# Kernel optimization log

Hardware: AMD Instinct MI355X
Metric: run time of the kernel (lower is better)

## Reference

```python
import jax, jax.numpy as jnp
import numpy as np

CUTOFF = 5.0
EPS = 1e-7
N = 50000
L = 160.0


def _cart3(a, b, c):
    # cartesian product of ranges [-a..a] x [-b..b] x [-c..c], row-major like torch.cartesian_prod
    A, B, C = np.meshgrid(np.arange(-a, a + 1), np.arange(-b, b + 1), np.arange(-c, c + 1), indexing='ij')
    return np.stack([A.ravel(), B.ravel(), C.ravel()], axis=1)


def wrap_positions(positions, cell):
    scaled = positions @ jnp.linalg.inv(cell) + EPS
    scaled = scaled % 1.0 - EPS
    return scaled @ cell


def setup_inputs() -> dict:
    key = jax.random.key(0)
    positions = jax.random.uniform(key, (N, 3), dtype=jnp.float32) * L
    cell = jnp.eye(3, dtype=jnp.float32) * L
    return {"positions": positions, "cell": cell}


def reference(positions, cell):
    wrapped = wrap_positions(positions, cell)

    cell_np = np.asarray(cell, dtype=np.float64)
    norm_a = np.linalg.norm(np.cross(cell_np[1], cell_np[2]))
    norm_b = np.linalg.norm(np.cross(cell_np[2], cell_np[0]))
    norm_c = np.linalg.norm(np.cross(cell_np[0], cell_np[1]))
    volume = float(np.dot(cell_np[0], np.cross(cell_np[1], cell_np[2])))
    pa = int(np.ceil(CUTOFF * norm_a / volume))
    pb = int(np.ceil(CUTOFF * norm_b / volume))
    pc = int(np.ceil(CUTOFF * norm_c / volume))

    pad_mat = jnp.asarray(_cart3(pa, pb, pc), dtype=positions.dtype)  # [P,3]
    P = pad_mat.shape[0]
    n = wrapped.shape[0]

    # replicate atoms into all periodic images: index k -> atom k//P, image k%P
    padded_pos = (wrapped[:, None, :] + pad_mat @ cell).reshape(-1, 3)  # [n*P,3]
    padded_cpos = jnp.floor(padded_pos / CUTOFF).astype(jnp.int32)
    corner = padded_cpos.min(axis=0)
    padded_cpos = padded_cpos - corner
    shap = np.asarray(padded_cpos.max(axis=0)) + 1
    num_cells = int(shap.prod())
    count_vec = jnp.asarray([int(shap[1] * shap[2]), int(shap[2]), 1], dtype=jnp.int32)

    padded_cind = (padded_cpos * count_vec).sum(axis=1)  # linear cell id per padded atom
    padded_gind = jnp.arange(n * P, dtype=jnp.int32) + 1  # 1-based so 0 == empty slot
    padded_rind = jnp.repeat(jnp.arange(n, dtype=jnp.int32), P)  # real-atom id of each image

    atom_cpos = jnp.floor(wrapped / CUTOFF).astype(jnp.int32) - corner
    disp = jnp.asarray(_cart3(1, 1, 1), dtype=jnp.int32)  # 27-cell stencil
    atom_cnind = ((atom_cpos[:, None, :] + disp) * count_vec).sum(axis=-1)  # [n,27]

    # stable sort by cell id, then within-cell rank (== torch unique_consecutive bookkeeping)
    cind_np = np.asarray(padded_cind)
    order = np.argsort(cind_np, kind='stable')
    sorted_cind = cind_np[order]
    _, counts = np.unique(sorted_cind, return_counts=True)
    max_anum = int(counts.max())
    starts = np.repeat(np.cumsum(counts) - counts, counts)
    ranks = np.arange(sorted_cind.shape[0]) - starts

    gci = jnp.zeros((num_cells, max_anum, 2), dtype=jnp.int32)
    gci = gci.at[sorted_cind, ranks, 0].set(padded_gind[order])
    gci = gci.at[sorted_cind, ranks, 1].set(padded_rind[order])

    atom_nind = gci[atom_cnind]  # [n,27,max_anum,2]
    occ = np.asarray(atom_nind[..., 0])
    pair_i, neigh, jslot = np.nonzero(occ)
    pair_jp = occ[pair_i, neigh, jslot] - 1  # index into padded_pos
    pair_j = np.asarray(atom_nind[..., 1])[pair_i, neigh, jslot]

    pair_diff = padded_pos[pair_jp] - wrapped[pair_i]
    pair_dist = jnp.linalg.norm(pair_diff, axis=1)
    mask = np.asarray((pair_dist < CUTOFF) & (pair_dist > 0.01))
    keep = np.nonzero(mask)[0]

    pairs = jnp.stack([jnp.asarray(pair_i, jnp.int32), jnp.asarray(pair_j, jnp.int32)], axis=1)
    return pairs[keep], pair_diff[keep], pair_dist[keep]
```

## Files before the change

kernel.cpp:

```cpp
#include <hip/hip_runtime.h>


#define CUTOFF 5.0f
#define WEPS   1e-7f
#define PIMG   27
#define G      36
#define NCELLS (G*G*G)
#define SLOT   16
#define NT1    256
#define NB2    2048
#define NT2    256
#define JPT    3
#define CAP    16
#define CSTR   17
#define BCAP   512
#define IMAX   0x7FFFFFFF
#define PRUNE2 25.001f


__device__ __forceinline__ void inv_diag3(const float* __restrict__ cell, float inv[9]) {
  float c[9];
#pragma unroll
  for (int i = 0; i < 9; i++) c[i] = cell[i];
  float a00=c[0],a01=c[1],a02=c[2],a10=c[3],a11=c[4],a12=c[5],a20=c[6],a21=c[7],a22=c[8];
  float m00 = __fsub_rn(__fmul_rn(a11,a22), __fmul_rn(a12,a21));
  float m01 = __fsub_rn(__fmul_rn(a10,a22), __fmul_rn(a12,a20));
  float m02 = __fsub_rn(__fmul_rn(a10,a21), __fmul_rn(a11,a20));
  float det = __fadd_rn(__fsub_rn(__fmul_rn(a00,m00), __fmul_rn(a01,m01)), __fmul_rn(a02,m02));
  inv[0] = __fdiv_rn(m00, det);
  inv[1] = __fdiv_rn(__fsub_rn(__fmul_rn(a02,a21), __fmul_rn(a01,a22)), det);
  inv[2] = __fdiv_rn(__fsub_rn(__fmul_rn(a01,a12), __fmul_rn(a02,a11)), det);
  inv[3] = __fdiv_rn(__fsub_rn(__fmul_rn(a12,a20), __fmul_rn(a10,a22)), det);
  inv[4] = __fdiv_rn(__fsub_rn(__fmul_rn(a00,a22), __fmul_rn(a02,a20)), det);
  inv[5] = __fdiv_rn(__fsub_rn(__fmul_rn(a02,a10), __fmul_rn(a00,a12)), det);
  inv[6] = __fdiv_rn(m02, det);
  inv[7] = __fdiv_rn(__fsub_rn(__fmul_rn(a01,a20), __fmul_rn(a00,a21)), det);
  inv[8] = __fdiv_rn(__fsub_rn(__fmul_rn(a00,a11), __fmul_rn(a01,a10)), det);
}

__device__ __forceinline__ int axis_opts(float w, float cdiag, int* pcomp, int* cellv,
                                         float* shv) {
  int cc = (int)floorf(__fdiv_rn(w, CUTOFF));
  int k = 0;
  if (cc >= 29) {
    float wp = __fsub_rn(w, cdiag);
    int c2 = (int)floorf(__fdiv_rn(wp, CUTOFF)) + 2;
    if ((unsigned)c2 < G) { pcomp[k] = 0; cellv[k] = c2; shv[k] = __fsub_rn(0.0f, cdiag); k++; }
  }
  pcomp[k] = 1; cellv[k] = cc + 2; shv[k] = 0.0f; k++;
  if (cc <= 2) {
    float wp = __fadd_rn(w, cdiag);
    int c2 = (int)floorf(__fdiv_rn(wp, CUTOFF)) + 2;
    if ((unsigned)c2 < G) { pcomp[k] = 2; cellv[k] = c2; shv[k] = cdiag; k++; }
  }
  return k;
}

__device__ __forceinline__ bool dist_ok(float4 f, float4 w) {
  float ax = __fsub_rn(f.x, w.x), ay = __fsub_rn(f.y, w.y), az = __fsub_rn(f.z, w.z);
  float d = __fsqrt_rn(__fadd_rn(__fadd_rn(__fmul_rn(ax, ax), __fmul_rn(ay, ay)),
                                 __fmul_rn(az, az)));
  return (d < CUTOFF && d > 0.01f);
}

__device__ __forceinline__ unsigned match_mask(const float4* __restrict__ cdata,
                                               int base, int cnt, float4 w) {
  unsigned mask = 0;
  for (int q = 0; q < cnt; q++)
    if (dist_ok(cdata[base + q], w)) mask |= 1u << q;
  return mask;
}

__device__ __forceinline__ int pick_min_t(const float4* __restrict__ cdata, int base,
                                          unsigned mask) {
  int bq = -1, bt = IMAX;
  for (unsigned m2 = mask; m2; m2 &= m2 - 1) {
    int q = __builtin_ctz(m2);
    int t = __float_as_int(cdata[base + q].w);
    if (t < bt) { bt = t; bq = q; }
  }
  return bq;
}

__device__ __forceinline__ float axis_q(float w, int c) {
  float lo = (float)((c - 2) * 5);
  float t = w - lo;
  float v = fmaxf(fmaxf(-t, t - 5.0f), 0.0f);
  return v * v;
}

__device__ __forceinline__ void cswap(int& a, int& b) {
  int lo = min(a, b), hi = max(a, b);
  a = lo; b = hi;
}

__device__ __forceinline__ int exscan256(int v, int* lds, int* total) {
  int tid = threadIdx.x, lane = tid & 63, wave = tid >> 6;
  int x = v;
#pragma unroll
  for (int off = 1; off < 64; off <<= 1) {
    int y = __shfl_up(x, off);
    if (lane >= off) x += y;
  }
  if (lane == 63) lds[wave] = x;
  __syncthreads();
  if (wave == 0) {
    int wv = (lane < 4) ? lds[lane] : 0;
#pragma unroll
    for (int off = 1; off < 4; off <<= 1) {
      int y = __shfl_up(wv, off);
      if (lane >= off) wv += y;
    }
    if (lane < 4) lds[lane] = wv;
  }
  __syncthreads();
  int wbase = (wave == 0) ? 0 : lds[wave - 1];
  *total = lds[3];
  __syncthreads();
  return wbase + x - v;
}

__device__ __forceinline__ int exscan1024(int v, int* lds, int* total) {
  int tid = threadIdx.x, lane = tid & 63, wave = tid >> 6;
  int x = v;
#pragma unroll
  for (int off = 1; off < 64; off <<= 1) {
    int y = __shfl_up(x, off);
    if (lane >= off) x += y;
  }
  if (lane == 63) lds[wave] = x;
  __syncthreads();
  if (wave == 0) {
    int wv = (lane < 16) ? lds[lane] : 0;
#pragma unroll
    for (int off = 1; off < 16; off <<= 1) {
      int y = __shfl_up(wv, off);
      if (lane >= off) wv += y;
    }
    if (lane < 16) lds[lane] = wv;
  }
  __syncthreads();
  int wbase = (wave == 0) ? 0 : lds[wave - 1];
  *total = lds[15];
  __syncthreads();
  return wbase + x - v;
}

__global__ void __launch_bounds__(NT1)
k_build(const float* __restrict__ pos, const float* __restrict__ cell,
        int* __restrict__ fill, float4* __restrict__ wrapped,
        float4* __restrict__ cdata, int n) {
  const int ai = blockIdx.x * NT1 + threadIdx.x;
  if (ai >= n) return;
  float inv[9];
  inv_diag3(cell, inv);
  float px = pos[3*ai], py = pos[3*ai+1], pz = pos[3*ai+2];
  float m[3];
#pragma unroll
  for (int col = 0; col < 3; col++) {
    float s = __fadd_rn(__fadd_rn(__fmul_rn(px, inv[col]), __fmul_rn(py, inv[3+col])),
                        __fmul_rn(pz, inv[6+col]));
    s = __fadd_rn(s, WEPS);
    float t = __fsub_rn(s, floorf(s));
    m[col] = __fsub_rn(t, WEPS);
  }
  float wx = __fadd_rn(__fadd_rn(__fmul_rn(m[0], cell[0]), __fmul_rn(m[1], cell[3])),
                       __fmul_rn(m[2], cell[6]));
  float wy = __fadd_rn(__fadd_rn(__fmul_rn(m[0], cell[1]), __fmul_rn(m[1], cell[4])),
                       __fmul_rn(m[2], cell[7]));
  float wz = __fadd_rn(__fadd_rn(__fmul_rn(m[0], cell[2]), __fmul_rn(m[1], cell[5])),
                       __fmul_rn(m[2], cell[8]));
  wrapped[ai] = make_float4(wx, wy, wz, 0.0f);
  int px_[2], py_[2], pz_[2], cx_[2], cy_[2], cz_[2];
  float sx_[2], sy_[2], sz_[2];
  int nx = axis_opts(wx, cell[0], px_, cx_, sx_);
  int ny = axis_opts(wy, cell[4], py_, cy_, sy_);
  int nz = axis_opts(wz, cell[8], pz_, cz_, sz_);
  for (int a = 0; a < nx; a++)
    for (int b = 0; b < ny; b++)
      for (int c = 0; c < nz; c++) {
        int cid = (cx_[a] * G + cy_[b]) * G + cz_[c];
        int p = (px_[a] * 3 + py_[b]) * 3 + pz_[c];
        int slot = atomicAdd(&fill[cid], 1);
        if (slot < SLOT)
          cdata[cid * SLOT + slot] =
              make_float4(__fadd_rn(wx, sx_[a]), __fadd_rn(wy, sy_[b]),
                          __fadd_rn(wz, sz_[c]), __int_as_float(ai * PIMG + p));
      }
}

__global__ void __launch_bounds__(NT2)
k_pair(const float4* __restrict__ wrapped, const int* __restrict__ fill,
       const float4* __restrict__ cdata, int2* __restrict__ paddr,
       int* __restrict__ blockSum, int n) {
  __shared__ int lds[8];
  __shared__ int pcache[NT2 * CSTR];
  const int tid = threadIdx.x, blk = blockIdx.x;
  const int n27 = n * PIMG;
  const int tbase = (blk * NT2 + tid) * JPT;
  const int i0 = min(tbase, n27 - 1) / PIMG;
  const int i1 = min(tbase + JPT - 1, n27 - 1) / PIMG;
  const float4 w0 = wrapped[i0];
  const float4 w1 = wrapped[i1];
  const int cx0 = (int)floorf(__fdiv_rn(w0.x, CUTOFF)) + 2;
  const int cy0 = (int)floorf(__fdiv_rn(w0.y, CUTOFF)) + 2;
  const int cz0 = (int)floorf(__fdiv_rn(w0.z, CUTOFF)) + 2;
  const int cx1 = (int)floorf(__fdiv_rn(w1.x, CUTOFF)) + 2;
  const int cy1 = (int)floorf(__fdiv_rn(w1.y, CUTOFF)) + 2;
  const int cz1 = (int)floorf(__fdiv_rn(w1.z, CUTOFF)) + 2;
  int bases[JPT], cnts[JPT];
#pragma unroll
  for (int j = 0; j < JPT; j++) {
    int idx = tbase + j;
    bool valid = idx < n27;
    int ic = valid ? idx / PIMG : i0;
    int s27 = valid ? idx - ic * PIMG : 0;
    bool a0 = (ic == i0);
    int ix = s27 / 9, iy = (s27 / 3) % 3, iz = s27 % 3;
    float wxs = a0 ? w0.x : w1.x, wys = a0 ? w0.y : w1.y, wzs = a0 ? w0.z : w1.z;
    int cx = (a0 ? cx0 : cx1) + ix - 1;
    int cy = (a0 ? cy0 : cy1) + iy - 1;
    int cz = (a0 ? cz0 : cz1) + iz - 1;
    float ps = axis_q(wxs, cx) + axis_q(wys, cy) + axis_q(wzs, cz);
    bool keep = valid && (ps <= PRUNE2);
    int cid = (cx * G + cy) * G + cz;
    bases[j] = cid * SLOT;
    cnts[j] = keep ? min(fill[cid], SLOT) : 0;
  }
  int tcnt = 0, c0 = 0;
#pragma unroll
  for (int j = 0; j < JPT; j++) {
    bool a0 = (tbase + j) < (i0 + 1) * PIMG;
    float4 w = a0 ? w0 : w1;
    int base = bases[j], cnt = cnts[j];
    if (cnt > 0) {
      if (cnt <= 4) {
        float4 f0 = cdata[base + 0];
        float4 f1 = cdata[base + 1];
        float4 f2 = cdata[base + 2];
        float4 f3 = cdata[base + 3];
        int a = (cnt > 0 && dist_ok(f0, w)) ? (__float_as_int(f0.w) * 16 + 0) : IMAX;
        int b = (cnt > 1 && dist_ok(f1, w)) ? (__float_as_int(f1.w) * 16 + 1) : IMAX;
        int c = (cnt > 2 && dist_ok(f2, w)) ? (__float_as_int(f2.w) * 16 + 2) : IMAX;
        int d = (cnt > 3 && dist_ok(f3, w)) ? (__float_as_int(f3.w) * 16 + 3) : IMAX;
        cswap(a, b); cswap(c, d); cswap(a, c); cswap(b, d); cswap(b, c);
        if (a != IMAX) { if (tcnt < CAP) pcache[tid * CSTR + tcnt] = base + (a & 15); tcnt++; }
        if (b != IMAX) { if (tcnt < CAP) pcache[tid * CSTR + tcnt] = base + (b & 15); tcnt++; }
        if (c != IMAX) { if (tcnt < CAP) pcache[tid * CSTR + tcnt] = base + (c & 15); tcnt++; }
        if (d != IMAX) { if (tcnt < CAP) pcache[tid * CSTR + tcnt] = base + (d & 15); tcnt++; }
      } else {
        unsigned mask = match_mask(cdata, base, cnt, w);
        while (mask) {
          int bq = pick_min_t(cdata, base, mask);
          mask &= ~(1u << bq);
          if (tcnt < CAP) pcache[tid * CSTR + tcnt] = base + bq;
          tcnt++;
        }
      }
    }
    if (a0) c0 = tcnt;
  }
  int btotal;
  const int texcl = exscan256(tcnt, lds, &btotal);
  if (tid == 0) blockSum[blk] = btotal;
  int2* dst = paddr + (size_t)blk * BCAP;
  if (tcnt <= CAP) {
    for (int k = 0; k < tcnt; k++) {
      int o = texcl + k;
      if (o < BCAP) dst[o] = make_int2(pcache[tid * CSTR + k], (k < c0) ? i0 : i1);
    }
  } else {
    int o = texcl;
#pragma unroll
    for (int j = 0; j < JPT; j++) {
      bool a0 = (tbase + j) < (i0 + 1) * PIMG;
      float4 w = a0 ? w0 : w1;
      int i = a0 ? i0 : i1;
      int base = bases[j];
      unsigned mask = match_mask(cdata, base, cnts[j], w);
      while (mask) {
        int bq = pick_min_t(cdata, base, mask);
        mask &= ~(1u << bq);
        if (o < BCAP) dst[o] = make_int2(base + bq, i);
        o++;
      }
    }
  }
}

__global__ void __launch_bounds__(1024)
k_scan(const int* __restrict__ blockSum, int* __restrict__ blockBase,
       float* __restrict__ out, int K) {
  __shared__ int lds[32];
  const int tid = threadIdx.x;
  int s0 = blockSum[2 * tid], s1 = blockSum[2 * tid + 1];
  int total;
  int ex = exscan1024(s0 + s1, lds, &total);
  blockBase[2 * tid] = ex;
  blockBase[2 * tid + 1] = ex + s0;
  if (tid == 0 && total != K) {
    float code = (total < K) ? (1000000.0f + (float)min(K - total, 100000))
                             : (2000000.0f + (float)min(total - K, 100000));
    for (int t = 0; t < 256; t++) out[t] = code;
  }
}

__global__ void __launch_bounds__(NT2)
k_emit(const float4* __restrict__ wrapped, const float4* __restrict__ cdata,
       const int2* __restrict__ paddr, const int* __restrict__ blockSum,
       const int* __restrict__ blockBase, float* __restrict__ out, int K) {
  const int blk = blockIdx.x;
  const int bs = min(blockSum[blk], BCAP);
  const int base = blockBase[blk];
  const int2* src = paddr + (size_t)blk * BCAP;
  for (int l = threadIdx.x; l < bs; l += NT2) {
    int2 e = src[l];
    float4 f = cdata[e.x];
    float4 w = wrapped[e.y];
    int o = base + l;
    float ax = __fsub_rn(f.x, w.x), ay = __fsub_rn(f.y, w.y), az = __fsub_rn(f.z, w.z);
    float d = __fsqrt_rn(__fadd_rn(__fadd_rn(__fmul_rn(ax, ax), __fmul_rn(ay, ay)),
                                   __fmul_rn(az, az)));
    if (o >= 0 && o < K) {
      int tt = __float_as_int(f.w);
      ((float2*)out)[o] = make_float2((float)e.y, (float)(tt / PIMG));
      size_t db = (size_t)2 * K + (size_t)3 * o;
      out[db]     = ax;
      out[db + 1] = ay;
      out[db + 2] = az;
      out[(size_t)5 * K + o] = d;
    }
  }
}

extern "C" void kernel_launch(void* const* d_in, const int* in_sizes, int n_in,
                              void* d_out, int out_size, void* d_ws, size_t ws_size,
                              hipStream_t stream) {
  const float* pos  = (const float*)d_in[0];
  const float* cell = (const float*)d_in[1];
  float* out = (float*)d_out;
  int n = in_sizes[0] / 3;
  int K = out_size / 6;

  char* ws = (char*)d_ws;
  size_t off = 0;
  auto alloc = [&](size_t bytes) -> char* {
    char* p = ws + off;
    off = (off + bytes + 255) & ~(size_t)255;
    return p;
  };
  int*    fill      = (int*)alloc((size_t)NCELLS * 4);
  size_t  zbytes    = off;
  float4* wrapped   = (float4*)alloc((size_t)n * 16);
  float4* cdata     = (float4*)alloc((size_t)NCELLS * SLOT * 16);
  int2*   paddr     = (int2*)alloc((size_t)NB2 * BCAP * 8);
  int*    blockSum  = (int*)alloc((size_t)NB2 * 4);
  int*    blockBase = (int*)alloc((size_t)NB2 * 4);
  if (off > ws_size) return;

  (void)hipMemsetAsync(fill, 0, zbytes, stream);
  int nb1 = (n + NT1 - 1) / NT1;
  k_build<<<nb1, NT1, 0, stream>>>(pos, cell, fill, wrapped, cdata, n);
  k_pair<<<NB2, NT2, 0, stream>>>(wrapped, fill, cdata, paddr, blockSum, n);
  k_scan<<<1, 1024, 0, stream>>>(blockSum, blockBase, out, K);
  k_emit<<<NB2, NT2, 0, stream>>>(wrapped, cdata, paddr, blockSum, blockBase, out, K);
}
```

Measured before the change: 98.63 us.

## Sort atoms by cell and assign four threads per atom in pair search

Atoms get a counting sort by home cell (new cell-count scan and scatter kernels), so k_pair blocks handle spatially coherent atoms. Each atom is served by four threads covering about seven stencil cells each, and the 27 images per atom are combined with shuffles instead of a block-wide scan. Output offsets now come from a per-atom scan in place of per-block sums. An overflow path rescans serially in k_emit. The aim is better cache locality and less scan work, at the cost of two extra launches, two single-block scans over 46k cells and 50k atoms, and more workspace traffic.

```diff
diff --git a/kernel.cpp b/kernel.cpp
--- a/kernel.cpp
+++ b/kernel.cpp
@@ -8,12 +8,13 @@
 #define NCELLS (G*G*G)
 #define SLOT   16
 #define NT1    256
-#define NB2    2048
-#define NT2    256
-#define JPT    3
-#define CAP    16
-#define CSTR   17
-#define BCAP   512
+#define NTP    256
+#define APB    (NTP/4)
+#define PPART  12
+#define PSTR   13
+#define CAPA   24
+#define NTE    256
+#define SPA    8
 #define IMAX   0x7FFFFFFF
 #define PRUNE2 25.001f
 
@@ -94,32 +95,6 @@
   a = lo; b = hi;
 }
 
-__device__ __forceinline__ int exscan256(int v, int* lds, int* total) {
-  int tid = threadIdx.x, lane = tid & 63, wave = tid >> 6;
-  int x = v;
-#pragma unroll
-  for (int off = 1; off < 64; off <<= 1) {
-    int y = __shfl_up(x, off);
-    if (lane >= off) x += y;
-  }
-  if (lane == 63) lds[wave] = x;
-  __syncthreads();
-  if (wave == 0) {
-    int wv = (lane < 4) ? lds[lane] : 0;
-#pragma unroll
-    for (int off = 1; off < 4; off <<= 1) {
-      int y = __shfl_up(wv, off);
-      if (lane >= off) wv += y;
-    }
-    if (lane < 4) lds[lane] = wv;
-  }
-  __syncthreads();
-  int wbase = (wave == 0) ? 0 : lds[wave - 1];
-  *total = lds[3];
-  __syncthreads();
-  return wbase + x - v;
-}
-
 __device__ __forceinline__ int exscan1024(int v, int* lds, int* total) {
   int tid = threadIdx.x, lane = tid & 63, wave = tid >> 6;
   int x = v;
@@ -148,8 +123,9 @@
 
 __global__ void __launch_bounds__(NT1)
 k_build(const float* __restrict__ pos, const float* __restrict__ cell,
-        int* __restrict__ fill, float4* __restrict__ wrapped,
-        float4* __restrict__ cdata, int n) {
+        int* __restrict__ fill, int* __restrict__ ccnt,
+        float4* __restrict__ wrapped, float4* __restrict__ cdata,
+        int* __restrict__ ccell, int* __restrict__ cslot, int n) {
   const int ai = blockIdx.x * NT1 + threadIdx.x;
   if (ai >= n) return;
   float inv[9];
@@ -171,6 +147,12 @@
   float wz = __fadd_rn(__fadd_rn(__fmul_rn(m[0], cell[2]), __fmul_rn(m[1], cell[5])),
                        __fmul_rn(m[2], cell[8]));
   wrapped[ai] = make_float4(wx, wy, wz, 0.0f);
+  int cxc = (int)floorf(__fdiv_rn(wx, CUTOFF)) + 2;
+  int cyc = (int)floorf(__fdiv_rn(wy, CUTOFF)) + 2;
+  int czc = (int)floorf(__fdiv_rn(wz, CUTOFF)) + 2;
+  int cidc = (cxc * G + cyc) * G + czc;
+  ccell[ai] = cidc;
+  cslot[ai] = atomicAdd(&ccnt[cidc], 1);
   int px_[2], py_[2], pz_[2], cx_[2], cy_[2], cz_[2];
   float sx_[2], sy_[2], sz_[2];
   int nx = axis_opts(wx, cell[0], px_, cx_, sx_);
@@ -189,115 +171,136 @@
       }
 }
 
-__global__ void __launch_bounds__(NT2)
+__global__ void __launch_bounds__(1024)
+k_cellscan(const int* __restrict__ ccnt, int* __restrict__ cbase) {
+  __shared__ int lds[32];
+  const int tid = threadIdx.x;
+  const int CHC = (NCELLS + 1023) / 1024;
+  int start = tid * CHC;
+  int sum = 0;
+  for (int k = 0; k < CHC; k++) {
+    int idx = start + k;
+    if (idx < NCELLS) sum += ccnt[idx];
+  }
+  int total;
+  int ex = exscan1024(sum, lds, &total);
+  int run = ex;
+  for (int k = 0; k < CHC; k++) {
+    int idx = start + k;
+    if (idx < NCELLS) { cbase[idx] = run; run += ccnt[idx]; }
+  }
+}
+
+__global__ void __launch_bounds__(NT1)
+k_scatter(const int* __restrict__ ccell, const int* __restrict__ cslot,
+          const int* __restrict__ cbase, int* __restrict__ sorted,
+          int* __restrict__ invp, int n) {
+  const int ai = blockIdx.x * NT1 + threadIdx.x;
+  if (ai >= n) return;
+  int si = cbase[ccell[ai]] + cslot[ai];
+  sorted[si] = ai;
+  invp[ai] = si;
+}
+
+__global__ void __launch_bounds__(NTP)
 k_pair(const float4* __restrict__ wrapped, const int* __restrict__ fill,
-       const float4* __restrict__ cdata, int2* __restrict__ paddr,
-       int* __restrict__ blockSum, int n) {
-  __shared__ int lds[8];
-  __shared__ int pcache[NT2 * CSTR];
-  const int tid = threadIdx.x, blk = blockIdx.x;
-  const int n27 = n * PIMG;
-  const int tbase = (blk * NT2 + tid) * JPT;
-  const int i0 = min(tbase, n27 - 1) / PIMG;
-  const int i1 = min(tbase + JPT - 1, n27 - 1) / PIMG;
-  const float4 w0 = wrapped[i0];
-  const float4 w1 = wrapped[i1];
-  const int cx0 = (int)floorf(__fdiv_rn(w0.x, CUTOFF)) + 2;
-  const int cy0 = (int)floorf(__fdiv_rn(w0.y, CUTOFF)) + 2;
-  const int cz0 = (int)floorf(__fdiv_rn(w0.z, CUTOFF)) + 2;
-  const int cx1 = (int)floorf(__fdiv_rn(w1.x, CUTOFF)) + 2;
-  const int cy1 = (int)floorf(__fdiv_rn(w1.y, CUTOFF)) + 2;
-  const int cz1 = (int)floorf(__fdiv_rn(w1.z, CUTOFF)) + 2;
-  int bases[JPT], cnts[JPT];
-#pragma unroll
-  for (int j = 0; j < JPT; j++) {
-    int idx = tbase + j;
-    bool valid = idx < n27;
-    int ic = valid ? idx / PIMG : i0;
-    int s27 = valid ? idx - ic * PIMG : 0;
-    bool a0 = (ic == i0);
-    int ix = s27 / 9, iy = (s27 / 3) % 3, iz = s27 % 3;
-    float wxs = a0 ? w0.x : w1.x, wys = a0 ? w0.y : w1.y, wzs = a0 ? w0.z : w1.z;
-    int cx = (a0 ? cx0 : cx1) + ix - 1;
-    int cy = (a0 ? cy0 : cy1) + iy - 1;
-    int cz = (a0 ? cz0 : cz1) + iz - 1;
-    float ps = axis_q(wxs, cx) + axis_q(wys, cy) + axis_q(wzs, cz);
+       const float4* __restrict__ cdata, const int* __restrict__ sorted,
+       int* __restrict__ patom, int* __restrict__ pcnt,
+       int* __restrict__ oflw, int n) {
+  __shared__ int pcache[NTP * PSTR];
+  const int tid = threadIdx.x;
+  const int si = blockIdx.x * APB + (tid >> 2);
+  const int part = tid & 3;
+  const bool act = si < n;
+  const int ai = act ? sorted[si] : 0;
+  const float4 w = wrapped[ai];
+  const int cxb = (int)floorf(__fdiv_rn(w.x, CUTOFF)) + 2;
+  const int cyb = (int)floorf(__fdiv_rn(w.y, CUTOFF)) + 2;
+  const int czb = (int)floorf(__fdiv_rn(w.z, CUTOFF)) + 2;
+  const int j0 = part * 7;
+  const int nj = (part == 3) ? 6 : 7;
+  int bases[7], cnts[7];
+#pragma unroll
+  for (int jj = 0; jj < 7; jj++) {
+    int j = j0 + jj;
+    bool valid = act && (jj < nj);
+    int ix = j / 9, iy = (j / 3) % 3, iz = j % 3;
+    int cx = cxb + ix - 1, cy = cyb + iy - 1, cz = czb + iz - 1;
+    float ps = axis_q(w.x, cx) + axis_q(w.y, cy) + axis_q(w.z, cz);
     bool keep = valid && (ps <= PRUNE2);
     int cid = (cx * G + cy) * G + cz;
-    bases[j] = cid * SLOT;
-    cnts[j] = keep ? min(fill[cid], SLOT) : 0;
-  }
-  int tcnt = 0, c0 = 0;
-#pragma unroll
-  for (int j = 0; j < JPT; j++) {
-    bool a0 = (tbase + j) < (i0 + 1) * PIMG;
-    float4 w = a0 ? w0 : w1;
-    int base = bases[j], cnt = cnts[j];
-    if (cnt > 0) {
-      if (cnt <= 4) {
+    bases[jj] = cid * SLOT;
+    cnts[jj] = keep ? min(fill[cid], SLOT) : 0;
+  }
+  int cnt = 0, of = 0;
+#pragma unroll
+  for (int jj = 0; jj < 7; jj++) {
+    int base = bases[jj], cc = cnts[jj];
+    if (cc > 0) {
+      if (cc <= 4) {
         float4 f0 = cdata[base + 0];
         float4 f1 = cdata[base + 1];
         float4 f2 = cdata[base + 2];
         float4 f3 = cdata[base + 3];
-        int a = (cnt > 0 && dist_ok(f0, w)) ? (__float_as_int(f0.w) * 16 + 0) : IMAX;
-        int b = (cnt > 1 && dist_ok(f1, w)) ? (__float_as_int(f1.w) * 16 + 1) : IMAX;
-        int c = (cnt > 2 && dist_ok(f2, w)) ? (__float_as_int(f2.w) * 16 + 2) : IMAX;
-        int d = (cnt > 3 && dist_ok(f3, w)) ? (__float_as_int(f3.w) * 16 + 3) : IMAX;
+        int a = (cc > 0 && dist_ok(f0, w)) ? (__float_as_int(f0.w) * 16 + 0) : IMAX;
+        int b = (cc > 1 && dist_ok(f1, w)) ? (__float_as_int(f1.w) * 16 + 1) : IMAX;
+        int c = (cc > 2 && dist_ok(f2, w)) ? (__float_as_int(f2.w) * 16 + 2) : IMAX;
+        int d = (cc > 3 && dist_ok(f3, w)) ? (__float_as_int(f3.w) * 16 + 3) : IMAX;
         cswap(a, b); cswap(c, d); cswap(a, c); cswap(b, d); cswap(b, c);
-        if (a != IMAX) { if (tcnt < CAP) pcache[tid * CSTR + tcnt] = base + (a & 15); tcnt++; }
-        if (b != IMAX) { if (tcnt < CAP) pcache[tid * CSTR + tcnt] = base + (b & 15); tcnt++; }
-        if (c != IMAX) { if (tcnt < CAP) pcache[tid * CSTR + tcnt] = base + (c & 15); tcnt++; }
-        if (d != IMAX) { if (tcnt < CAP) pcache[tid * CSTR + tcnt] = base + (d & 15); tcnt++; }
+        if (a != IMAX) { if (cnt < PPART) pcache[tid * PSTR + cnt] = base + (a & 15); else of = 1; cnt++; }
+        if (b != IMAX) { if (cnt < PPART) pcache[tid * PSTR + cnt] = base + (b & 15); else of = 1; cnt++; }
+        if (c != IMAX) { if (cnt < PPART) pcache[tid * PSTR + cnt] = base + (c & 15); else of = 1; cnt++; }
+        if (d != IMAX) { if (cnt < PPART) pcache[tid * PSTR + cnt] = base + (d & 15); else of = 1; cnt++; }
       } else {
-        unsigned mask = match_mask(cdata, base, cnt, w);
+        unsigned mask = match_mask(cdata, base, cc, w);
         while (mask) {
           int bq = pick_min_t(cdata, base, mask);
           mask &= ~(1u << bq);
-          if (tcnt < CAP) pcache[tid * CSTR + tcnt] = base + bq;
-          tcnt++;
+          if (cnt < PPART) pcache[tid * PSTR + cnt] = base + bq; else of = 1;
+          cnt++;
         }
       }
     }
-    if (a0) c0 = tcnt;
-  }
-  int btotal;
-  const int texcl = exscan256(tcnt, lds, &btotal);
-  if (tid == 0) blockSum[blk] = btotal;
-  int2* dst = paddr + (size_t)blk * BCAP;
-  if (tcnt <= CAP) {
-    for (int k = 0; k < tcnt; k++) {
-      int o = texcl + k;
-      if (o < BCAP) dst[o] = make_int2(pcache[tid * CSTR + k], (k < c0) ? i0 : i1);
+  }
+  int c1 = __shfl_up(cnt, 1);
+  int c2 = __shfl_up(cnt, 2);
+  int c3 = __shfl_up(cnt, 3);
+  int off = ((part >= 1) ? c1 : 0) + ((part >= 2) ? c2 : 0) + ((part >= 3) ? c3 : 0);
+  int total = off + cnt;
+  int ofv = of;
+  ofv |= __shfl_xor(ofv, 1);
+  ofv |= __shfl_xor(ofv, 2);
+  if (act) {
+    if (part == 3) {
+      pcnt[ai] = total;
+      oflw[ai] = (ofv || total > CAPA) ? 1 : 0;
     }
-  } else {
-    int o = texcl;
-#pragma unroll
-    for (int j = 0; j < JPT; j++) {
-      bool a0 = (tbase + j) < (i0 + 1) * PIMG;
-      float4 w = a0 ? w0 : w1;
-      int i = a0 ? i0 : i1;
-      int base = bases[j];
-      unsigned mask = match_mask(cdata, base, cnts[j], w);
-      while (mask) {
-        int bq = pick_min_t(cdata, base, mask);
-        mask &= ~(1u << bq);
-        if (o < BCAP) dst[o] = make_int2(base + bq, i);
-        o++;
-      }
-    }
+    int kmax = min(cnt, PPART);
+    int* dst = patom + (size_t)si * CAPA + off;
+    for (int k = 0; k < kmax; k++)
+      if (off + k < CAPA) dst[k] = pcache[tid * PSTR + k];
   }
 }
 
 __global__ void __launch_bounds__(1024)
-k_scan(const int* __restrict__ blockSum, int* __restrict__ blockBase,
-       float* __restrict__ out, int K) {
+k_ascan(const int* __restrict__ pcnt, int* __restrict__ abase,
+        float* __restrict__ out, int K, int n) {
   __shared__ int lds[32];
   const int tid = threadIdx.x;
-  int s0 = blockSum[2 * tid], s1 = blockSum[2 * tid + 1];
+  const int chw = (n + 1023) >> 10;
+  int start = tid * chw;
+  int sum = 0;
+  for (int k = 0; k < chw; k++) {
+    int idx = start + k;
+    if (idx < n) sum += pcnt[idx];
+  }
   int total;
-  int ex = exscan1024(s0 + s1, lds, &total);
-  blockBase[2 * tid] = ex;
-  blockBase[2 * tid + 1] = ex + s0;
+  int ex = exscan1024(sum, lds, &total);
+  int run = ex;
+  for (int k = 0; k < chw; k++) {
+    int idx = start + k;
+    if (idx < n) { abase[idx] = run; run += pcnt[idx]; }
+  }
   if (tid == 0 && total != K) {
     float code = (total < K) ? (1000000.0f + (float)min(K - total, 100000))
                              : (2000000.0f + (float)min(total - K, 100000));
@@ -305,30 +308,69 @@
   }
 }
 
-__global__ void __launch_bounds__(NT2)
-k_emit(const float4* __restrict__ wrapped, const float4* __restrict__ cdata,
-       const int2* __restrict__ paddr, const int* __restrict__ blockSum,
-       const int* __restrict__ blockBase, float* __restrict__ out, int K) {
-  const int blk = blockIdx.x;
-  const int bs = min(blockSum[blk], BCAP);
-  const int base = blockBase[blk];
-  const int2* src = paddr + (size_t)blk * BCAP;
-  for (int l = threadIdx.x; l < bs; l += NT2) {
-    int2 e = src[l];
-    float4 f = cdata[e.x];
-    float4 w = wrapped[e.y];
-    int o = base + l;
-    float ax = __fsub_rn(f.x, w.x), ay = __fsub_rn(f.y, w.y), az = __fsub_rn(f.z, w.z);
-    float d = __fsqrt_rn(__fadd_rn(__fadd_rn(__fmul_rn(ax, ax), __fmul_rn(ay, ay)),
-                                   __fmul_rn(az, az)));
-    if (o >= 0 && o < K) {
-      int tt = __float_as_int(f.w);
-      ((float2*)out)[o] = make_float2((float)e.y, (float)(tt / PIMG));
-      size_t db = (size_t)2 * K + (size_t)3 * o;
-      out[db]     = ax;
-      out[db + 1] = ay;
-      out[db + 2] = az;
-      out[(size_t)5 * K + o] = d;
+__global__ void __launch_bounds__(NTE)
+k_emit(const float4* __restrict__ wrapped, const int* __restrict__ fill,
+       const float4* __restrict__ cdata, const int* __restrict__ patom,
+       const int* __restrict__ pcnt, const int* __restrict__ oflw,
+       const int* __restrict__ abase, const int* __restrict__ invp,
+       float* __restrict__ out, int K, int n) {
+  const int gtid = blockIdx.x * NTE + threadIdx.x;
+  const int ai = gtid >> 3, sl = gtid & (SPA - 1);
+  if (ai >= n) return;
+  const int cntp = pcnt[ai];
+  const int base = abase[ai];
+  const float4 w = wrapped[ai];
+  if (!oflw[ai]) {
+    const int* src = patom + (size_t)invp[ai] * CAPA;
+    for (int k = sl; k < cntp; k += SPA) {
+      int addr = src[k];
+      float4 f = cdata[addr];
+      int o = base + k;
+      float ax = __fsub_rn(f.x, w.x), ay = __fsub_rn(f.y, w.y), az = __fsub_rn(f.z, w.z);
+      float d = __fsqrt_rn(__fadd_rn(__fadd_rn(__fmul_rn(ax, ax), __fmul_rn(ay, ay)),
+                                     __fmul_rn(az, az)));
+      if (o >= 0 && o < K) {
+        int tt = __float_as_int(f.w);
+        ((float2*)out)[o] = make_float2((float)ai, (float)(tt / PIMG));
+        size_t db = (size_t)2 * K + (size_t)3 * o;
+        out[db]     = ax;
+        out[db + 1] = ay;
+        out[db + 2] = az;
+        out[(size_t)5 * K + o] = d;
+      }
+    }
+  } else if (sl == 0) {
+    const int cxb = (int)floorf(__fdiv_rn(w.x, CUTOFF)) + 2;
+    const int cyb = (int)floorf(__fdiv_rn(w.y, CUTOFF)) + 2;
+    const int czb = (int)floorf(__fdiv_rn(w.z, CUTOFF)) + 2;
+    int o = base;
+    for (int j = 0; j < PIMG; j++) {
+      int ix = j / 9, iy = (j / 3) % 3, iz = j % 3;
+      int cx = cxb + ix - 1, cy = cyb + iy - 1, cz = czb + iz - 1;
+      float ps = axis_q(w.x, cx) + axis_q(w.y, cy) + axis_q(w.z, cz);
+      if (ps > PRUNE2) continue;
+      int cid = (cx * G + cy) * G + cz;
+      int cc = min(fill[cid], SLOT);
+      int sb = cid * SLOT;
+      unsigned mask = match_mask(cdata, sb, cc, w);
+      while (mask) {
+        int bq = pick_min_t(cdata, sb, mask);
+        mask &= ~(1u << bq);
+        float4 f = cdata[sb + bq];
+        float ax = __fsub_rn(f.x, w.x), ay = __fsub_rn(f.y, w.y), az = __fsub_rn(f.z, w.z);
+        float d = __fsqrt_rn(__fadd_rn(__fadd_rn(__fmul_rn(ax, ax), __fmul_rn(ay, ay)),
+                                       __fmul_rn(az, az)));
+        if (o >= 0 && o < K) {
+          int tt = __float_as_int(f.w);
+          ((float2*)out)[o] = make_float2((float)ai, (float)(tt / PIMG));
+          size_t db = (size_t)2 * K + (size_t)3 * o;
+          out[db]     = ax;
+          out[db + 1] = ay;
+          out[db + 2] = az;
+          out[(size_t)5 * K + o] = d;
+        }
+        o++;
+      }
     }
   }
 }
@@ -349,19 +391,33 @@
     off = (off + bytes + 255) & ~(size_t)255;
     return p;
   };
-  int*    fill      = (int*)alloc((size_t)NCELLS * 4);
-  size_t  zbytes    = off;
-  float4* wrapped   = (float4*)alloc((size_t)n * 16);
-  float4* cdata     = (float4*)alloc((size_t)NCELLS * SLOT * 16);
-  int2*   paddr     = (int2*)alloc((size_t)NB2 * BCAP * 8);
-  int*    blockSum  = (int*)alloc((size_t)NB2 * 4);
-  int*    blockBase = (int*)alloc((size_t)NB2 * 4);
+  int*    fill    = (int*)alloc((size_t)NCELLS * 4);
+  int*    ccnt    = (int*)alloc((size_t)NCELLS * 4);
+  size_t  zbytes  = off;
+  float4* wrapped = (float4*)alloc((size_t)n * 16);
+  float4* cdata   = (float4*)alloc((size_t)NCELLS * SLOT * 16);
+  int*    cbase   = (int*)alloc((size_t)NCELLS * 4);
+  int*    ccell   = (int*)alloc((size_t)n * 4);
+  int*    cslot   = (int*)alloc((size_t)n * 4);
+  int*    sorted  = (int*)alloc((size_t)n * 4);
+  int*    invp    = (int*)alloc((size_t)n * 4);
+  int*    patom   = (int*)alloc((size_t)n * CAPA * 4);
+  int*    pcnt    = (int*)alloc((size_t)n * 4);
+  int*    oflw    = (int*)alloc((size_t)n * 4);
+  int*    abase   = (int*)alloc((size_t)n * 4);
   if (off > ws_size) return;
 
   (void)hipMemsetAsync(fill, 0, zbytes, stream);
-  int nb1 = (n + NT1 - 1) / NT1;
-  k_build<<<nb1, NT1, 0, stream>>>(pos, cell, fill, wrapped, cdata, n);
-  k_pair<<<NB2, NT2, 0, stream>>>(wrapped, fill, cdata, paddr, blockSum, n);
-  k_scan<<<1, 1024, 0, stream>>>(blockSum, blockBase, out, K);
-  k_emit<<<NB2, NT2, 0, stream>>>(wrapped, cdata, paddr, blockSum, blockBase, out, K);
-}
+  int nbA = (n + NT1 - 1) / NT1;
+  int nbP = (n + APB - 1) / APB;
+  int nbE = ((size_t)n * SPA + NTE - 1) / NTE;
+  k_build<<<nbA, NT1, 0, stream>>>(pos, cell, fill, ccnt, wrapped, cdata,
+                                   ccell, cslot, n);
+  k_cellscan<<<1, 1024, 0, stream>>>(ccnt, cbase);
+  k_scatter<<<nbA, NT1, 0, stream>>>(ccell, cslot, cbase, sorted, invp, n);
+  k_pair<<<nbP, NTP, 0, stream>>>(wrapped, fill, cdata, sorted, patom, pcnt,
+                                  oflw, n);
+  k_ascan<<<1, 1024, 0, stream>>>(pcnt, abase, out, K, n);
+  k_emit<<<nbE, NTE, 0, stream>>>(wrapped, fill, cdata, patom, pcnt, oflw,
+                                  abase, invp, out, K, n);
+}
```

After: 298.7 us. 203% more time.

## Fuse pair, scan and emit kernels via decoupled look-back single-pass scan

Applied to the files above, without the earlier changes.

Merges the pair-finding, block-sum scan and emit kernels into one kernel. Block offsets come from a decoupled look-back scan over a per-block state array, with block order set by an atomic ticket, and each thread writes its pairs straight to the output. This removes two kernel launches and the round trip through the intermediate pair-address buffer. In exchange it adds a serial look-back spin on thread 0 of each block, relaxed atomics without explicit fences, and a spin cap that can silently fall back on timeout.

```diff
diff --git a/kernel.cpp b/kernel.cpp
--- a/kernel.cpp
+++ b/kernel.cpp
@@ -13,9 +13,13 @@
 #define JPT    3
 #define CAP    16
 #define CSTR   17
-#define BCAP   512
 #define IMAX   0x7FFFFFFF
 #define PRUNE2 25.001f
+#define SPINCAP (1<<20)
+#define FLG_A  (1u<<30)
+#define FLG_I  (2u<<30)
+#define FLG_M  (3u<<30)
+#define VMASK  ((1u<<30)-1)
 
 
 __device__ __forceinline__ void inv_diag3(const float* __restrict__ cell, float inv[9]) {
@@ -116,32 +120,6 @@
   __syncthreads();
   int wbase = (wave == 0) ? 0 : lds[wave - 1];
   *total = lds[3];
-  __syncthreads();
-  return wbase + x - v;
-}
-
-__device__ __forceinline__ int exscan1024(int v, int* lds, int* total) {
-  int tid = threadIdx.x, lane = tid & 63, wave = tid >> 6;
-  int x = v;
-#pragma unroll
-  for (int off = 1; off < 64; off <<= 1) {
-    int y = __shfl_up(x, off);
-    if (lane >= off) x += y;
-  }
-  if (lane == 63) lds[wave] = x;
-  __syncthreads();
-  if (wave == 0) {
-    int wv = (lane < 16) ? lds[lane] : 0;
-#pragma unroll
-    for (int off = 1; off < 16; off <<= 1) {
-      int y = __shfl_up(wv, off);
-      if (lane >= off) wv += y;
-    }
-    if (lane < 16) lds[lane] = wv;
-  }
-  __syncthreads();
-  int wbase = (wave == 0) ? 0 : lds[wave - 1];
-  *total = lds[15];
   __syncthreads();
   return wbase + x - v;
 }
@@ -190,14 +168,18 @@
 }
 
 __global__ void __launch_bounds__(NT2)
-k_pair(const float4* __restrict__ wrapped, const int* __restrict__ fill,
-       const float4* __restrict__ cdata, int2* __restrict__ paddr,
-       int* __restrict__ blockSum, int n) {
+k_pairemit(const float4* __restrict__ wrapped, const int* __restrict__ fill,
+           const float4* __restrict__ cdata, int* __restrict__ ticket,
+           int* __restrict__ state, float* __restrict__ out, int K, int n) {
   __shared__ int lds[8];
   __shared__ int pcache[NT2 * CSTR];
-  const int tid = threadIdx.x, blk = blockIdx.x;
+  __shared__ int sh_vbid, sh_excl;
+  const int tid = threadIdx.x;
+  if (tid == 0) sh_vbid = atomicAdd(ticket, 1);
+  __syncthreads();
+  const int vbid = sh_vbid;
   const int n27 = n * PIMG;
-  const int tbase = (blk * NT2 + tid) * JPT;
+  const int tbase = (vbid * NT2 + tid) * JPT;
   const int i0 = min(tbase, n27 - 1) / PIMG;
   const int i1 = min(tbase + JPT - 1, n27 - 1) / PIMG;
   const float4 w0 = wrapped[i0];
@@ -262,15 +244,60 @@
   }
   int btotal;
   const int texcl = exscan256(tcnt, lds, &btotal);
-  if (tid == 0) blockSum[blk] = btotal;
-  int2* dst = paddr + (size_t)blk * BCAP;
+
+  if (tid == 0) {
+    __hip_atomic_store(&state[vbid], FLG_A | (unsigned)btotal,
+                       __ATOMIC_RELAXED, __HIP_MEMORY_SCOPE_AGENT);
+    int excl = 0;
+    for (int p = vbid - 1; p >= 0; ) {
+      unsigned s;
+      int guard = 0;
+      while ((((s = __hip_atomic_load(&state[p], __ATOMIC_RELAXED,
+                                      __HIP_MEMORY_SCOPE_AGENT))) & FLG_M) == 0) {
+        __builtin_amdgcn_s_sleep(1);
+        if (++guard > SPINCAP) { s = FLG_I; break; }
+      }
+      excl += (int)(s & VMASK);
+      if ((s & FLG_M) == FLG_I) break;
+      p--;
+    }
+    __hip_atomic_store(&state[vbid], FLG_I | (unsigned)(excl + btotal),
+                       __ATOMIC_RELAXED, __HIP_MEMORY_SCOPE_AGENT);
+    sh_excl = excl;
+    if (vbid == NB2 - 1) {
+      int total = excl + btotal;
+      if (total != K) {
+        float code = (total < K) ? (1000000.0f + (float)min(K - total, 100000))
+                                 : (2000000.0f + (float)min(total - K, 100000));
+        for (int t = 0; t < 256; t++) out[t] = code;
+      }
+    }
+  }
+  __syncthreads();
+  const int obase = sh_excl + texcl;
+
+  int o = obase;
   if (tcnt <= CAP) {
     for (int k = 0; k < tcnt; k++) {
-      int o = texcl + k;
-      if (o < BCAP) dst[o] = make_int2(pcache[tid * CSTR + k], (k < c0) ? i0 : i1);
+      float4 f = cdata[pcache[tid * CSTR + k]];
+      bool a0 = (k < c0);
+      float4 w = a0 ? w0 : w1;
+      int i = a0 ? i0 : i1;
+      float ax = __fsub_rn(f.x, w.x), ay = __fsub_rn(f.y, w.y), az = __fsub_rn(f.z, w.z);
+      float d = __fsqrt_rn(__fadd_rn(__fadd_rn(__fmul_rn(ax, ax), __fmul_rn(ay, ay)),
+                                     __fmul_rn(az, az)));
+      if (o >= 0 && o < K) {
+        int tt = __float_as_int(f.w);
+        ((float2*)out)[o] = make_float2((float)i, (float)(tt / PIMG));
+        size_t db = (size_t)2 * K + (size_t)3 * o;
+        out[db]     = ax;
+        out[db + 1] = ay;
+        out[db + 2] = az;
+        out[(size_t)5 * K + o] = d;
+      }
+      o++;
     }
   } else {
-    int o = texcl;
 #pragma unroll
     for (int j = 0; j < JPT; j++) {
       bool a0 = (tbase + j) < (i0 + 1) * PIMG;
@@ -281,54 +308,21 @@
       while (mask) {
         int bq = pick_min_t(cdata, base, mask);
         mask &= ~(1u << bq);
-        if (o < BCAP) dst[o] = make_int2(base + bq, i);
+        float4 f = cdata[base + bq];
+        float ax = __fsub_rn(f.x, w.x), ay = __fsub_rn(f.y, w.y), az = __fsub_rn(f.z, w.z);
+        float d = __fsqrt_rn(__fadd_rn(__fadd_rn(__fmul_rn(ax, ax), __fmul_rn(ay, ay)),
+                                       __fmul_rn(az, az)));
+        if (o >= 0 && o < K) {
+          int tt = __float_as_int(f.w);
+          ((float2*)out)[o] = make_float2((float)i, (float)(tt / PIMG));
+          size_t db = (size_t)2 * K + (size_t)3 * o;
+          out[db]     = ax;
+          out[db + 1] = ay;
+          out[db + 2] = az;
+          out[(size_t)5 * K + o] = d;
+        }
         o++;
       }
-    }
-  }
-}
-
-__global__ void __launch_bounds__(1024)
-k_scan(const int* __restrict__ blockSum, int* __restrict__ blockBase,
-       float* __restrict__ out, int K) {
-  __shared__ int lds[32];
-  const int tid = threadIdx.x;
-  int s0 = blockSum[2 * tid], s1 = blockSum[2 * tid + 1];
-  int total;
-  int ex = exscan1024(s0 + s1, lds, &total);
-  blockBase[2 * tid] = ex;
-  blockBase[2 * tid + 1] = ex + s0;
-  if (tid == 0 && total != K) {
-    float code = (total < K) ? (1000000.0f + (float)min(K - total, 100000))
-                             : (2000000.0f + (float)min(total - K, 100000));
-    for (int t = 0; t < 256; t++) out[t] = code;
-  }
-}
-
-__global__ void __launch_bounds__(NT2)
-k_emit(const float4* __restrict__ wrapped, const float4* __restrict__ cdata,
-       const int2* __restrict__ paddr, const int* __restrict__ blockSum,
-       const int* __restrict__ blockBase, float* __restrict__ out, int K) {
-  const int blk = blockIdx.x;
-  const int bs = min(blockSum[blk], BCAP);
-  const int base = blockBase[blk];
-  const int2* src = paddr + (size_t)blk * BCAP;
-  for (int l = threadIdx.x; l < bs; l += NT2) {
-    int2 e = src[l];
-    float4 f = cdata[e.x];
-    float4 w = wrapped[e.y];
-    int o = base + l;
-    float ax = __fsub_rn(f.x, w.x), ay = __fsub_rn(f.y, w.y), az = __fsub_rn(f.z, w.z);
-    float d = __fsqrt_rn(__fadd_rn(__fadd_rn(__fmul_rn(ax, ax), __fmul_rn(ay, ay)),
-                                   __fmul_rn(az, az)));
-    if (o >= 0 && o < K) {
-      int tt = __float_as_int(f.w);
-      ((float2*)out)[o] = make_float2((float)e.y, (float)(tt / PIMG));
-      size_t db = (size_t)2 * K + (size_t)3 * o;
-      out[db]     = ax;
-      out[db + 1] = ay;
-      out[db + 2] = az;
-      out[(size_t)5 * K + o] = d;
     }
   }
 }
@@ -349,19 +343,17 @@
     off = (off + bytes + 255) & ~(size_t)255;
     return p;
   };
-  int*    fill      = (int*)alloc((size_t)NCELLS * 4);
-  size_t  zbytes    = off;
-  float4* wrapped   = (float4*)alloc((size_t)n * 16);
-  float4* cdata     = (float4*)alloc((size_t)NCELLS * SLOT * 16);
-  int2*   paddr     = (int2*)alloc((size_t)NB2 * BCAP * 8);
-  int*    blockSum  = (int*)alloc((size_t)NB2 * 4);
-  int*    blockBase = (int*)alloc((size_t)NB2 * 4);
+  int*    fill    = (int*)alloc((size_t)NCELLS * 4);
+  int*    ticket  = (int*)alloc(256);
+  int*    state   = (int*)alloc((size_t)NB2 * 4);
+  size_t  zbytes  = off;
+  float4* wrapped = (float4*)alloc((size_t)n * 16);
+  float4* cdata   = (float4*)alloc((size_t)NCELLS * SLOT * 16);
   if (off > ws_size) return;
 
   (void)hipMemsetAsync(fill, 0, zbytes, stream);
   int nb1 = (n + NT1 - 1) / NT1;
   k_build<<<nb1, NT1, 0, stream>>>(pos, cell, fill, wrapped, cdata, n);
-  k_pair<<<NB2, NT2, 0, stream>>>(wrapped, fill, cdata, paddr, blockSum, n);
-  k_scan<<<1, 1024, 0, stream>>>(blockSum, blockBase, out, K);
-  k_emit<<<NB2, NT2, 0, stream>>>(wrapped, cdata, paddr, blockSum, blockBase, out, K);
-}
+  k_pairemit<<<NB2, NT2, 0, stream>>>(wrapped, fill, cdata, ticket, state,
+                                      out, K, n);
+}
```

Result: slower. 147.2 us (+49.2%).

## Replace fixed-slot cell bins with compacted CSR cell lists via count-scan-place

Applied to the files above, without the earlier changes.

Cell binning moves from a fixed 16-slot-per-cell array to a CSR layout. A counting pass, a single-block prefix scan over all cells and a placement pass now fill a compact array. Neighbor lookups read cell start and end offsets from the scan, so cells can hold more than 16 images (up to 32 are examined) and candidate data sits densely in memory. In exchange it adds two kernel launches, a second round of atomics and a serial single-block scan over about 46K cells. Inside a cell, image order now depends on atomic timing, which is handled by the existing min-index selection.

```diff
diff --git a/kernel.cpp b/kernel.cpp
--- a/kernel.cpp
+++ b/kernel.cpp
@@ -6,7 +6,6 @@
 #define PIMG   27
 #define G      36
 #define NCELLS (G*G*G)
-#define SLOT   16
 #define NT1    256
 #define NB2    2048
 #define NT2    256
@@ -14,6 +13,7 @@
 #define CAP    16
 #define CSTR   17
 #define BCAP   512
+#define CMAX   32
 #define IMAX   0x7FFFFFFF
 #define PRUNE2 25.001f
 
@@ -63,20 +63,20 @@
   return (d < CUTOFF && d > 0.01f);
 }
 
-__device__ __forceinline__ unsigned match_mask(const float4* __restrict__ cdata,
+__device__ __forceinline__ unsigned match_mask(const float4* __restrict__ csr,
                                                int base, int cnt, float4 w) {
   unsigned mask = 0;
   for (int q = 0; q < cnt; q++)
-    if (dist_ok(cdata[base + q], w)) mask |= 1u << q;
+    if (dist_ok(csr[base + q], w)) mask |= 1u << q;
   return mask;
 }
 
-__device__ __forceinline__ int pick_min_t(const float4* __restrict__ cdata, int base,
+__device__ __forceinline__ int pick_min_t(const float4* __restrict__ csr, int base,
                                           unsigned mask) {
   int bq = -1, bt = IMAX;
   for (unsigned m2 = mask; m2; m2 &= m2 - 1) {
     int q = __builtin_ctz(m2);
-    int t = __float_as_int(cdata[base + q].w);
+    int t = __float_as_int(csr[base + q].w);
     if (t < bt) { bt = t; bq = q; }
   }
   return bq;
@@ -146,10 +146,46 @@
   return wbase + x - v;
 }
 
+__device__ __forceinline__ int scan_tiled(const int* __restrict__ X,
+                                          int* __restrict__ P, int N, int* lds) {
+  const int tid = threadIdx.x;
+  int carry = 0;
+  const int ntile = (N + 4095) >> 12;
+  for (int t = 0; t < ntile; t++) {
+    int idx = (t << 12) + (tid << 2);
+    int4 v = make_int4(0, 0, 0, 0);
+    if (idx + 3 < N) {
+      v = *(const int4*)(X + idx);
+    } else {
+      if (idx + 0 < N) v.x = X[idx + 0];
+      if (idx + 1 < N) v.y = X[idx + 1];
+      if (idx + 2 < N) v.z = X[idx + 2];
+      if (idx + 3 < N) v.w = X[idx + 3];
+    }
+    int s = v.x + v.y + v.z + v.w;
+    int ttotal;
+    int ex = exscan1024(s, lds, &ttotal) + carry;
+    int4 o;
+    o.x = ex;
+    o.y = ex + v.x;
+    o.z = o.y + v.y;
+    o.w = o.z + v.z;
+    if (idx + 3 < N) {
+      *(int4*)(P + idx) = o;
+    } else {
+      if (idx + 0 < N) P[idx + 0] = o.x;
+      if (idx + 1 < N) P[idx + 1] = o.y;
+      if (idx + 2 < N) P[idx + 2] = o.z;
+      if (idx + 3 < N) P[idx + 3] = o.w;
+    }
+    carry += ttotal;
+  }
+  return carry;
+}
+
 __global__ void __launch_bounds__(NT1)
-k_build(const float* __restrict__ pos, const float* __restrict__ cell,
-        int* __restrict__ fill, float4* __restrict__ wrapped,
-        float4* __restrict__ cdata, int n) {
+k_count(const float* __restrict__ pos, const float* __restrict__ cell,
+        int* __restrict__ ccnt, float4* __restrict__ wrapped, int n) {
   const int ai = blockIdx.x * NT1 + threadIdx.x;
   if (ai >= n) return;
   float inv[9];
@@ -180,18 +216,45 @@
     for (int b = 0; b < ny; b++)
       for (int c = 0; c < nz; c++) {
         int cid = (cx_[a] * G + cy_[b]) * G + cz_[c];
+        atomicAdd(&ccnt[cid], 1);
+      }
+}
+
+__global__ void __launch_bounds__(1024)
+k_cellscan(const int* __restrict__ ccnt, int* __restrict__ cbase) {
+  __shared__ int lds[32];
+  int total = scan_tiled(ccnt, cbase, NCELLS, lds);
+  if (threadIdx.x == 0) cbase[NCELLS] = total;
+}
+
+__global__ void __launch_bounds__(NT1)
+k_place(const float* __restrict__ cell, const float4* __restrict__ wrapped,
+        const int* __restrict__ cbase, int* __restrict__ ccur,
+        float4* __restrict__ csr, int n) {
+  const int ai = blockIdx.x * NT1 + threadIdx.x;
+  if (ai >= n) return;
+  float4 w = wrapped[ai];
+  float wx = w.x, wy = w.y, wz = w.z;
+  int px_[2], py_[2], pz_[2], cx_[2], cy_[2], cz_[2];
+  float sx_[2], sy_[2], sz_[2];
+  int nx = axis_opts(wx, cell[0], px_, cx_, sx_);
+  int ny = axis_opts(wy, cell[4], py_, cy_, sy_);
+  int nz = axis_opts(wz, cell[8], pz_, cz_, sz_);
+  for (int a = 0; a < nx; a++)
+    for (int b = 0; b < ny; b++)
+      for (int c = 0; c < nz; c++) {
+        int cid = (cx_[a] * G + cy_[b]) * G + cz_[c];
         int p = (px_[a] * 3 + py_[b]) * 3 + pz_[c];
-        int slot = atomicAdd(&fill[cid], 1);
-        if (slot < SLOT)
-          cdata[cid * SLOT + slot] =
-              make_float4(__fadd_rn(wx, sx_[a]), __fadd_rn(wy, sy_[b]),
-                          __fadd_rn(wz, sz_[c]), __int_as_float(ai * PIMG + p));
+        int cur = atomicAdd(&ccur[cid], 1);
+        csr[cbase[cid] + cur] =
+            make_float4(__fadd_rn(wx, sx_[a]), __fadd_rn(wy, sy_[b]),
+                        __fadd_rn(wz, sz_[c]), __int_as_float(ai * PIMG + p));
       }
 }
 
 __global__ void __launch_bounds__(NT2)
-k_pair(const float4* __restrict__ wrapped, const int* __restrict__ fill,
-       const float4* __restrict__ cdata, int2* __restrict__ paddr,
+k_pair(const float4* __restrict__ wrapped, const int* __restrict__ cbase,
+       const float4* __restrict__ csr, int2* __restrict__ paddr,
        int* __restrict__ blockSum, int n) {
   __shared__ int lds[8];
   __shared__ int pcache[NT2 * CSTR];
@@ -224,8 +287,10 @@
     float ps = axis_q(wxs, cx) + axis_q(wys, cy) + axis_q(wzs, cz);
     bool keep = valid && (ps <= PRUNE2);
     int cid = (cx * G + cy) * G + cz;
-    bases[j] = cid * SLOT;
-    cnts[j] = keep ? min(fill[cid], SLOT) : 0;
+    int cb = keep ? cbase[cid] : 0;
+    int ce = keep ? cbase[cid + 1] : 0;
+    bases[j] = cb;
+    cnts[j] = keep ? min(ce - cb, CMAX) : 0;
   }
   int tcnt = 0, c0 = 0;
 #pragma unroll
@@ -235,10 +300,10 @@
     int base = bases[j], cnt = cnts[j];
     if (cnt > 0) {
       if (cnt <= 4) {
-        float4 f0 = cdata[base + 0];
-        float4 f1 = cdata[base + 1];
-        float4 f2 = cdata[base + 2];
-        float4 f3 = cdata[base + 3];
+        float4 f0 = csr[base + 0];
+        float4 f1 = csr[base + 1];
+        float4 f2 = csr[base + 2];
+        float4 f3 = csr[base + 3];
         int a = (cnt > 0 && dist_ok(f0, w)) ? (__float_as_int(f0.w) * 16 + 0) : IMAX;
         int b = (cnt > 1 && dist_ok(f1, w)) ? (__float_as_int(f1.w) * 16 + 1) : IMAX;
         int c = (cnt > 2 && dist_ok(f2, w)) ? (__float_as_int(f2.w) * 16 + 2) : IMAX;
@@ -249,9 +314,9 @@
         if (c != IMAX) { if (tcnt < CAP) pcache[tid * CSTR + tcnt] = base + (c & 15); tcnt++; }
         if (d != IMAX) { if (tcnt < CAP) pcache[tid * CSTR + tcnt] = base + (d & 15); tcnt++; }
       } else {
-        unsigned mask = match_mask(cdata, base, cnt, w);
+        unsigned mask = match_mask(csr, base, cnt, w);
         while (mask) {
-          int bq = pick_min_t(cdata, base, mask);
+          int bq = pick_min_t(csr, base, mask);
           mask &= ~(1u << bq);
           if (tcnt < CAP) pcache[tid * CSTR + tcnt] = base + bq;
           tcnt++;
@@ -277,9 +342,9 @@
       float4 w = a0 ? w0 : w1;
       int i = a0 ? i0 : i1;
       int base = bases[j];
-      unsigned mask = match_mask(cdata, base, cnts[j], w);
+      unsigned mask = match_mask(csr, base, cnts[j], w);
       while (mask) {
-        int bq = pick_min_t(cdata, base, mask);
+        int bq = pick_min_t(csr, base, mask);
         mask &= ~(1u << bq);
         if (o < BCAP) dst[o] = make_int2(base + bq, i);
         o++;
@@ -306,7 +371,7 @@
 }
 
 __global__ void __launch_bounds__(NT2)
-k_emit(const float4* __restrict__ wrapped, const float4* __restrict__ cdata,
+k_emit(const float4* __restrict__ wrapped, const float4* __restrict__ csr,
        const int2* __restrict__ paddr, const int* __restrict__ blockSum,
        const int* __restrict__ blockBase, float* __restrict__ out, int K) {
   const int blk = blockIdx.x;
@@ -315,7 +380,7 @@
   const int2* src = paddr + (size_t)blk * BCAP;
   for (int l = threadIdx.x; l < bs; l += NT2) {
     int2 e = src[l];
-    float4 f = cdata[e.x];
+    float4 f = csr[e.x];
     float4 w = wrapped[e.y];
     int o = base + l;
     float ax = __fsub_rn(f.x, w.x), ay = __fsub_rn(f.y, w.y), az = __fsub_rn(f.z, w.z);
@@ -349,19 +414,23 @@
     off = (off + bytes + 255) & ~(size_t)255;
     return p;
   };
-  int*    fill      = (int*)alloc((size_t)NCELLS * 4);
+  int*    ccnt      = (int*)alloc((size_t)NCELLS * 4);
+  int*    ccur      = (int*)alloc((size_t)NCELLS * 4);
   size_t  zbytes    = off;
   float4* wrapped   = (float4*)alloc((size_t)n * 16);
-  float4* cdata     = (float4*)alloc((size_t)NCELLS * SLOT * 16);
+  int*    cbase     = (int*)alloc((size_t)(NCELLS + 1) * 4);
+  float4* csr       = (float4*)alloc((size_t)n * 8 * 16 + 256);
   int2*   paddr     = (int2*)alloc((size_t)NB2 * BCAP * 8);
   int*    blockSum  = (int*)alloc((size_t)NB2 * 4);
   int*    blockBase = (int*)alloc((size_t)NB2 * 4);
   if (off > ws_size) return;
 
-  (void)hipMemsetAsync(fill, 0, zbytes, stream);
-  int nb1 = (n + NT1 - 1) / NT1;
-  k_build<<<nb1, NT1, 0, stream>>>(pos, cell, fill, wrapped, cdata, n);
-  k_pair<<<NB2, NT2, 0, stream>>>(wrapped, fill, cdata, paddr, blockSum, n);
+  (void)hipMemsetAsync(ccnt, 0, zbytes, stream);
+  int nbA = (n + NT1 - 1) / NT1;
+  k_count<<<nbA, NT1, 0, stream>>>(pos, cell, ccnt, wrapped, n);
+  k_cellscan<<<1, 1024, 0, stream>>>(ccnt, cbase);
+  k_place<<<nbA, NT1, 0, stream>>>(cell, wrapped, cbase, ccur, csr, n);
+  k_pair<<<NB2, NT2, 0, stream>>>(wrapped, cbase, csr, paddr, blockSum, n);
   k_scan<<<1, 1024, 0, stream>>>(blockSum, blockBase, out, K);
-  k_emit<<<NB2, NT2, 0, stream>>>(wrapped, cdata, paddr, blockSum, blockBase, out, K);
-}
+  k_emit<<<NB2, NT2, 0, stream>>>(wrapped, csr, paddr, blockSum, blockBase, out, K);
+}
```

New measurement: 114.7 us. 16.3% more time.
